# Performance work log

Hardware: AMD Instinct MI355X
Metric: run time of the kernel (lower is better)

The kernel has to match this reference:

```python
import jax, jax.numpy as jnp
import numpy as np

N_ML, N_MM, L = 128, 8192, 60.0

def _half_shifts():
    # torchani _get_shifts half-shift enumeration for num_repeats=(1,1,1)
    r, o, m = [1], [0], [-1]
    def cp(a, b, c):
        return [(x, y, z) for x in a for y in b for z in c]
    combos = (cp(r, r, r) + cp(r, r, o) + cp(r, r, m)
              + cp(r, o, r) + cp(r, o, o) + cp(r, o, m)
              + cp(r, m, r) + cp(r, m, o) + cp(r, m, m)
              + cp(o, r, r) + cp(o, r, o) + cp(o, r, m)
              + cp(o, o, r))
    return np.array(combos, dtype=np.int32)  # (13, 3)

def setup_inputs() -> dict:
    key = jax.random.key(0)
    positions = jax.random.uniform(key, (N_ML + N_MM, 3), dtype=jnp.float32) * L
    cell = jnp.eye(3, dtype=jnp.float32) * L
    cutoffs = jnp.array([10.0, 14.0], dtype=jnp.float32)
    shifts = jnp.asarray(_half_shifts())              # (S=13, 3) int32
    ml_idx = jnp.arange(N_ML, dtype=jnp.int32)        # fragment 0 atoms
    mm_idx = jnp.arange(N_ML, N_ML + N_MM, dtype=jnp.int32)  # fragment 1 atoms
    return {"positions": positions, "cell": cell, "cutoffs": cutoffs,
            "shifts": shifts, "ml_idx": ml_idx, "mm_idx": mm_idx}

def reference(positions, cell, cutoffs, shifts, ml_idx, mm_idx):
    n_ml, n_mm = ml_idx.shape[0], mm_idx.shape[0]
    S = shifts.shape[0]
    # center image (zero shift) + periodic half-shifts -> (S+1, 3)
    shift_frac = jnp.concatenate(
        [jnp.zeros((1, 3), positions.dtype), shifts.astype(positions.dtype)], axis=0)
    shift_vec = shift_frac @ cell                     # (S+1, 3) cartesian
    # cartesian product ML x MM (matches torch.cartesian_prod ordering: sorted by i)
    pi = jnp.broadcast_to(ml_idx[:, None], (n_ml, n_mm)).reshape(-1)  # (P0,)
    pj = jnp.broadcast_to(mm_idx[None, :], (n_ml, n_mm)).reshape(-1)  # (P0,)
    # Rij = pos[i] - pos[j] + shift @ cell over all images: (S+1, P0, 3)
    Rij = positions[pi][None, :, :] - positions[pj][None, :, :] + shift_vec[:, None, :]
    d2 = jnp.sum(Rij * Rij, axis=-1).reshape(-1)      # (P,) P=(S+1)*P0
    P = d2.shape[0]
    pi_all = jnp.broadcast_to(pi[None, :], (S + 1, pi.shape[0])).reshape(-1)
    pj_all = jnp.broadcast_to(pj[None, :], (S + 1, pj.shape[0])).reshape(-1)
    sf_all = jnp.broadcast_to(shift_frac[:, None, :], (S + 1, pi.shape[0], 3)).reshape(-1, 3)
    # bi-directional duplication: bi_offset = cat((-seg_offset, seg_offset))
    idx_i = jnp.concatenate([pi_all, pj_all])          # (2P,)
    idx_j = jnp.concatenate([pj_all, pi_all])          # (2P,)
    offsets_frac = jnp.concatenate([-sf_all, sf_all], axis=0)  # (2P, 3)
    offsets_cart = offsets_frac @ cell                 # (2P, 3), seg_offset @ cell
    d2_full = jnp.concatenate([d2, d2])                # |Rij| symmetric under i<->j
    # per-cutoff in-range masks (fixed-shape stand-in for dynamic index compaction)
    masks = d2_full[None, :] < (cutoffs ** 2)[:, None]  # (n_cutoffs, 2P) bool
    return idx_i, idx_j, offsets_cart, d2_full, masks
```

## Files before the change

kernel.cpp:

```cpp
#include <hip/hip_runtime.h>
#include <stdint.h>

typedef float f4 __attribute__((ext_vector_type(4)));

__device__ __forceinline__ f4 rot3(float x, float y, float z, int t) {
    float a0 = (t == 0) ? x : ((t == 1) ? y : z);
    float a1 = (t == 0) ? y : ((t == 1) ? z : x);
    float a2 = (t == 0) ? z : ((t == 1) ? x : y);
    f4 r = {a0, a1, a2, a0};
    return r;
}

__global__ __launch_bounds__(256) void nl_kernel(
    const float* __restrict__ pos,
    const float* __restrict__ cell,
    const float* __restrict__ cutoffs,
    const int*   __restrict__ shifts,
    const int*   __restrict__ ml_idx,
    const int*   __restrict__ mm_idx,
    float* __restrict__ out,
    int n_mm, int P0, int P)
{
    int tid = blockIdx.x * blockDim.x + threadIdx.x;
    int p = tid << 2;
    if (p >= P) return;

    int s     = p / P0;
    int a     = p - s * P0;
    int i_idx = a / n_mm;
    int j0    = a - i_idx * n_mm;

    int pi = ml_idx[i_idx];
    float xi = pos[3 * pi + 0], yi = pos[3 * pi + 1], zi = pos[3 * pi + 2];

    int sx = 0, sy = 0, sz = 0;
    if (s > 0) {
        sx = shifts[3 * (s - 1) + 0];
        sy = shifts[3 * (s - 1) + 1];
        sz = shifts[3 * (s - 1) + 2];
    }
    float fx = (float)sx, fy = (float)sy, fz = (float)sz;
    float svx = __fadd_rn(__fadd_rn(__fmul_rn(fx, cell[0]), __fmul_rn(fy, cell[3])), __fmul_rn(fz, cell[6]));
    float svy = __fadd_rn(__fadd_rn(__fmul_rn(fx, cell[1]), __fmul_rn(fy, cell[4])), __fmul_rn(fz, cell[7]));
    float svz = __fadd_rn(__fadd_rn(__fmul_rn(fx, cell[2]), __fmul_rn(fy, cell[5])), __fmul_rn(fz, cell[8]));

    float c0 = __fmul_rn(cutoffs[0], cutoffs[0]);
    float c1 = __fmul_rn(cutoffs[1], cutoffs[1]);

    float fI = (float)pi;
    f4 vI = {fI, fI, fI, fI};
    f4 vJ, vD, vM0, vM1;

    int4 pj4 = *(const int4*)(mm_idx + j0);
    int pjs[4] = {pj4.x, pj4.y, pj4.z, pj4.w};
#pragma unroll
    for (int k = 0; k < 4; ++k) {
        int pj = pjs[k];
        float xj = pos[3 * pj + 0], yj = pos[3 * pj + 1], zj = pos[3 * pj + 2];
        float dx = __fadd_rn(__fsub_rn(xi, xj), svx);
        float dy = __fadd_rn(__fsub_rn(yi, yj), svy);
        float dz = __fadd_rn(__fsub_rn(zi, zj), svz);
        float d2 = __fadd_rn(__fadd_rn(__fmul_rn(dx, dx), __fmul_rn(dy, dy)), __fmul_rn(dz, dz));
        vJ[k]  = (float)pj;
        vD[k]  = d2;
        vM0[k] = (d2 < c0) ? 1.0f : 0.0f;
        vM1[k] = (d2 < c1) ? 1.0f : 0.0f;
    }

    size_t Pz = (size_t)P;
    size_t pp = (size_t)p;
    *(f4*)(out + 0 * Pz + pp)  = vI;
    *(f4*)(out + 1 * Pz + pp)  = vJ;
    *(f4*)(out + 2 * Pz + pp)  = vJ;
    *(f4*)(out + 3 * Pz + pp)  = vI;
    *(f4*)(out + 10 * Pz + pp) = vD;
    *(f4*)(out + 11 * Pz + pp) = vD;
    *(f4*)(out + 12 * Pz + pp) = vM0;
    *(f4*)(out + 13 * Pz + pp) = vM0;
    *(f4*)(out + 14 * Pz + pp) = vM1;
    *(f4*)(out + 15 * Pz + pp) = vM1;

    int lane = (int)(threadIdx.x & 63);
    size_t pw = pp - (size_t)(lane << 2);
    float nx = -svx, ny = -svy, nz = -svz;
    float* nb = out + 4 * Pz + 3 * pw;
    float* qb = out + 7 * Pz + 3 * pw;

    if (pw + 256 <= (size_t)P) {
#pragma unroll
        for (int c = 0; c < 3; ++c) {
            int t = (lane + c) % 3;
            *(f4*)(nb + c * 256 + 4 * lane) = rot3(nx, ny, nz, t);
            *(f4*)(qb + c * 256 + 4 * lane) = rot3(svx, svy, svz, t);
        }
    } else {
        float* n0 = out + 4 * Pz + 3 * pp;
        float* q0 = out + 7 * Pz + 3 * pp;
#pragma unroll
        for (int r = 0; r < 4; ++r) {
            n0[3*r+0] = nx;  n0[3*r+1] = ny;  n0[3*r+2] = nz;
            q0[3*r+0] = svx; q0[3*r+1] = svy; q0[3*r+2] = svz;
        }
    }
}

extern "C" void kernel_launch(void* const* d_in, const int* in_sizes, int n_in,
                              void* d_out, int out_size, void* d_ws, size_t ws_size,
                              hipStream_t stream) {
    const float* pos    = (const float*)d_in[0];
    const float* cell   = (const float*)d_in[1];
    const float* cut    = (const float*)d_in[2];
    const int*   shifts = (const int*)d_in[3];
    const int*   ml     = (const int*)d_in[4];
    const int*   mm     = (const int*)d_in[5];

    int n_ml = in_sizes[4];
    int n_mm = in_sizes[5];
    int S    = in_sizes[3] / 3;
    int P0   = n_ml * n_mm;
    int P    = (S + 1) * P0;

    int threads = P / 4;
    int grid = (threads + 255) / 256;
    nl_kernel<<<grid, 256, 0, stream>>>(pos, cell, cut, shifts, ml, mm,
                                        (float*)d_out, n_mm, P0, P);
}
```

Measured before the change: 909.8 us.

## Split output writing into per-section blocks on a 2D grid

Adds a kernel that launches one grid row per output section (16 sections) and lets each block write 4096 contiguous elements of a single section. The goal is fully coalesced, contiguous stores per block instead of each thread scattering to ten separate sections. The trade-off is recomputing distances separately for the d2 and mask sections (six times in total) and reloading mm_idx and positions in each block. The old kernel is kept as a fallback when sizes are not multiples of 4096.

```diff
diff --git a/kernel.cpp b/kernel.cpp
--- a/kernel.cpp
+++ b/kernel.cpp
@@ -9,6 +9,112 @@
     float a2 = (t == 0) ? z : ((t == 1) ? x : y);
     f4 r = {a0, a1, a2, a0};
     return r;
+}
+
+__device__ __forceinline__ void shift_vec_for(
+    int s, const int* __restrict__ shifts, const float* __restrict__ cell,
+    float& svx, float& svy, float& svz)
+{
+    int sx = 0, sy = 0, sz = 0;
+    if (s > 0) {
+        sx = shifts[3 * (s - 1) + 0];
+        sy = shifts[3 * (s - 1) + 1];
+        sz = shifts[3 * (s - 1) + 2];
+    }
+    float fx = (float)sx, fy = (float)sy, fz = (float)sz;
+    svx = __fadd_rn(__fadd_rn(__fmul_rn(fx, cell[0]), __fmul_rn(fy, cell[3])), __fmul_rn(fz, cell[6]));
+    svy = __fadd_rn(__fadd_rn(__fmul_rn(fx, cell[1]), __fmul_rn(fy, cell[4])), __fmul_rn(fz, cell[7]));
+    svz = __fadd_rn(__fadd_rn(__fmul_rn(fx, cell[2]), __fmul_rn(fy, cell[5])), __fmul_rn(fz, cell[8]));
+}
+
+__global__ __launch_bounds__(256) void nl_sections(
+    const float* __restrict__ pos,
+    const float* __restrict__ cell,
+    const float* __restrict__ cutoffs,
+    const int*   __restrict__ shifts,
+    const int*   __restrict__ ml_idx,
+    const int*   __restrict__ mm_idx,
+    float* __restrict__ out,
+    int n_mm, int P0, int P)
+{
+    const int sec  = blockIdx.y;
+    const int tid  = threadIdx.x;
+    const int base = blockIdx.x << 12;
+    float* __restrict__ dst =
+        out + (size_t)sec * (size_t)P + (size_t)base + ((size_t)tid << 2);
+
+    if (sec >= 4 && sec <= 9) {
+        const int o0     = (sec - 4) * P + base;
+        const int threeP = 3 * P;
+        const bool neg   = (o0 < threeP);
+        const int  oo    = neg ? o0 : (o0 - threeP);
+        const int  s     = oo / (3 * P0);
+        float svx, svy, svz;
+        shift_vec_for(s, shifts, cell, svx, svy, svz);
+        if (neg) { svx = -svx; svy = -svy; svz = -svz; }
+        const int t0 = (oo + (tid << 2)) % 3;
+#pragma unroll
+        for (int w = 0; w < 4; ++w) {
+            int t = t0 + w;
+            if (t >= 3) t -= 3;
+            if (t >= 3) t -= 3;
+            *(f4*)(dst + (w << 10)) = rot3(svx, svy, svz, t);
+        }
+        return;
+    }
+
+    const int s     = base / P0;
+    const int a     = base - s * P0;
+    const int i_idx = a / n_mm;
+    const int j0    = a - i_idx * n_mm;
+    const int pi    = ml_idx[i_idx];
+
+    if (sec == 0 || sec == 3) {
+        const float fI = (float)pi;
+        const f4 v = {fI, fI, fI, fI};
+#pragma unroll
+        for (int w = 0; w < 4; ++w) *(f4*)(dst + (w << 10)) = v;
+        return;
+    }
+
+    if (sec == 1 || sec == 2) {
+#pragma unroll
+        for (int w = 0; w < 4; ++w) {
+            int4 pj4 = *(const int4*)(mm_idx + j0 + (w << 10) + (tid << 2));
+            f4 v = {(float)pj4.x, (float)pj4.y, (float)pj4.z, (float)pj4.w};
+            *(f4*)(dst + (w << 10)) = v;
+        }
+        return;
+    }
+
+    float svx, svy, svz;
+    shift_vec_for(s, shifts, cell, svx, svy, svz);
+    const float xi = pos[3 * pi + 0];
+    const float yi = pos[3 * pi + 1];
+    const float zi = pos[3 * pi + 2];
+    const bool is_mask = (sec >= 12);
+    float cut = 0.0f;
+    if (is_mask) {
+        float c = (sec >= 14) ? cutoffs[1] : cutoffs[0];
+        cut = __fmul_rn(c, c);
+    }
+#pragma unroll
+    for (int w = 0; w < 4; ++w) {
+        int4 pj4 = *(const int4*)(mm_idx + j0 + (w << 10) + (tid << 2));
+        int pjs[4] = {pj4.x, pj4.y, pj4.z, pj4.w};
+        f4 v;
+#pragma unroll
+        for (int k = 0; k < 4; ++k) {
+            int pj = pjs[k];
+            float xj = pos[3 * pj + 0], yj = pos[3 * pj + 1], zj = pos[3 * pj + 2];
+            float dx = __fadd_rn(__fsub_rn(xi, xj), svx);
+            float dy = __fadd_rn(__fsub_rn(yi, yj), svy);
+            float dz = __fadd_rn(__fsub_rn(zi, zj), svz);
+            float d2 = __fadd_rn(__fadd_rn(__fmul_rn(dx, dx), __fmul_rn(dy, dy)), __fmul_rn(dz, dz));
+            v[k] = is_mask ? ((d2 < cut) ? 1.0f : 0.0f) : d2;
+        }
+        *(f4*)(dst + (w << 10)) = v;
+    }
 }
 
 __global__ __launch_bounds__(256) void nl_kernel(
@@ -33,16 +139,8 @@
     int pi = ml_idx[i_idx];
     float xi = pos[3 * pi + 0], yi = pos[3 * pi + 1], zi = pos[3 * pi + 2];
 
-    int sx = 0, sy = 0, sz = 0;
-    if (s > 0) {
-        sx = shifts[3 * (s - 1) + 0];
-        sy = shifts[3 * (s - 1) + 1];
-        sz = shifts[3 * (s - 1) + 2];
-    }
-    float fx = (float)sx, fy = (float)sy, fz = (float)sz;
-    float svx = __fadd_rn(__fadd_rn(__fmul_rn(fx, cell[0]), __fmul_rn(fy, cell[3])), __fmul_rn(fz, cell[6]));
-    float svy = __fadd_rn(__fadd_rn(__fmul_rn(fx, cell[1]), __fmul_rn(fy, cell[4])), __fmul_rn(fz, cell[7]));
-    float svz = __fadd_rn(__fadd_rn(__fmul_rn(fx, cell[2]), __fmul_rn(fy, cell[5])), __fmul_rn(fz, cell[8]));
+    float svx, svy, svz;
+    shift_vec_for(s, shifts, cell, svx, svy, svz);
 
     float c0 = __fmul_rn(cutoffs[0], cutoffs[0]);
     float c1 = __fmul_rn(cutoffs[1], cutoffs[1]);
@@ -120,8 +218,17 @@
     int P0   = n_ml * n_mm;
     int P    = (S + 1) * P0;
 
-    int threads = P / 4;
-    int grid = (threads + 255) / 256;
-    nl_kernel<<<grid, 256, 0, stream>>>(pos, cell, cut, shifts, ml, mm,
-                                        (float*)d_out, n_mm, P0, P);
-}
+    bool fast = (n_mm % 4096 == 0) && (P0 % 4096 == 0) && (P % 4096 == 0)
+                && (P <= 0x7fffffff / 6);
+
+    if (fast) {
+        dim3 grid(P >> 12, 16);
+        nl_sections<<<grid, 256, 0, stream>>>(pos, cell, cut, shifts, ml, mm,
+                                              (float*)d_out, n_mm, P0, P);
+    } else {
+        int threads = (P + 3) / 4;
+        int grid = (threads + 255) / 256;
+        nl_kernel<<<grid, 256, 0, stream>>>(pos, cell, cut, shifts, ml, mm,
+                                            (float*)d_out, n_mm, P0, P);
+    }
+}
```

New measurement: 916.5 us. About the same (+0.7%).
